# Performance work log

Hardware: AMD Instinct MI355X
Metric: run time of the kernel (lower is better)

Reference implementation:

```python
import jax, jax.numpy as jnp
import numpy as np

N = 3072
FEAT = 128
E = 24576


def setup_inputs() -> dict:
    key = jax.random.key(0)
    k1, k2, k3, k4 = jax.random.split(key, 4)
    x = jax.random.normal(k1, (N, FEAT), dtype=jnp.float32)
    edge_index = jax.random.randint(k2, (2, E), 0, N, dtype=jnp.int32)
    batch = jnp.zeros((N,), dtype=jnp.int32)
    # lin: Linear(2*FEAT, 1)
    w = jax.random.normal(k3, (2 * FEAT,), dtype=jnp.float32) / np.sqrt(2 * FEAT)
    b = jax.random.normal(k4, (), dtype=jnp.float32) * 0.01
    return {"x": x, "edge_index": edge_index, "batch": batch, "w": w, "b": b}


def _cc_labels(adj):
    """Connected-component labels via min-label propagation + pointer jumping.
    Labels equal the minimum node index of each component, so ranking them by
    value reproduces scipy's first-occurrence component ordering."""
    n = adj.shape[0]
    adj = jax.lax.stop_gradient(adj)

    def body(state):
        labels, _ = state
        neigh = jnp.where(adj > 0, labels[None, :], n).min(axis=1)  # [n]
        new = jnp.minimum(labels, neigh)
        new = jnp.minimum(new, new[new])  # pointer jumping
        return new, jnp.any(new != labels)

    labels, _ = jax.lax.while_loop(lambda s: s[1], body,
                                   (jnp.arange(n), jnp.array(True)))
    return labels


def reference(x, edge_index, batch, w, b):
    n, f = x.shape
    idx = jnp.arange(n)
    src, dst = edge_index[0], edge_index[1]
    # undirected: duplicate each edge in both directions (coalesce in the
    # original dedups; dense scatter-set below is equivalent since duplicate
    # (u,v) edges get identical scores)
    s2 = jnp.concatenate([src, dst])
    d2 = jnp.concatenate([dst, src])
    # per-edge raw score: lin(concat(x[u], x[v]))  ->  tanh
    e = jnp.tanh(x[s2] @ w[:f] + x[d2] @ w[f:] + b)  # [2E]

    zero = jnp.zeros((n, n), dtype=x.dtype)
    A = zero.at[s2, d2].set(1.0).at[idx, idx].set(0.0)   # self-loops removed
    S = zero.at[s2, d2].set(e).at[idx, idx].set(0.0)
    contract = (e > 0.0).astype(x.dtype)                 # tanh -> threshold 0
    A_c = zero.at[s2, d2].max(contract).at[idx, idx].set(0.0)

    labels = _cc_labels(A_c)                             # min-node-index labels
    roots = (labels == idx).astype(jnp.int32)
    cluster = (jnp.cumsum(roots) - 1)[labels]            # consecutive 0..K-1
    C = jax.nn.one_hot(cluster, n, dtype=x.dtype)        # [n, n] (padded to n)

    single = (A_c.sum(axis=1) + A_c.sum(axis=0)) == 0    # isolated under contraction
    S = S.at[idx, idx].set(single.astype(x.dtype))

    X_new = (S @ C).T @ x                                # [n(padK), f]
    A_new = (C.T @ A @ C).at[idx, idx].set(0.0)          # dense coarsened adjacency
    new_batch = jnp.zeros((n,), dtype=batch.dtype).at[cluster].max(batch)
    return X_new, A_new, new_batch, cluster
```

## Files before the change

kernel.cpp:

```cpp
#include <hip/hip_runtime.h>
#include <math.h>

#define N 3072
#define FEAT 128
#define NE 24576
#define PSTRIDE 64
#define EPT 24
#define NBLK 256
#define DOTB 768
#define OUTZ4 2459136
#define OUTZB 2402
#define WSZ4 1540
#define WSZB 2

__device__ __forceinline__ void wave_agg_add(bool valid, int key, float val,
                                             float* base, int stride, int off) {
    int lane = threadIdx.x & 63;
    unsigned long long active = __ballot(valid ? 1 : 0);
    while (active) {
        int leader = __ffsll(active) - 1;
        int lkey = __shfl(key, leader);
        bool mine = valid && (key == lkey);
        unsigned long long grp = __ballot(mine ? 1 : 0);
        float v = mine ? val : 0.0f;
        #pragma unroll
        for (int o = 32; o; o >>= 1) v += __shfl_xor(v, o);
        if (lane == leader)
            atomicAdd(&base[(size_t)lkey * stride + off], v);
        active &= ~grp;
    }
}

__device__ __forceinline__ void gsync(int* bar, int* lgen) {
    __syncthreads();
    if (threadIdx.x == 0) {
        __threadfence();
        int g = ++(*lgen);
        if (atomicAdd(&bar[0], 1) == (int)gridDim.x - 1) {
            __hip_atomic_store(&bar[0], 0, __ATOMIC_RELAXED, __HIP_MEMORY_SCOPE_AGENT);
            __threadfence();
            atomicAdd(&bar[1], 1);
        } else {
            while (__hip_atomic_load(&bar[1], __ATOMIC_RELAXED,
                                     __HIP_MEMORY_SCOPE_AGENT) < g)
                __builtin_amdgcn_s_sleep(8);
        }
        __threadfence();
    } else {
        ++(*lgen);
    }
    __syncthreads();
}

__global__ void k_init(const float* __restrict__ x, const float* __restrict__ w,
                       float* __restrict__ a, float* __restrict__ c,
                       float4* __restrict__ zout, float4* __restrict__ zws) {
    int b = blockIdx.x, t = threadIdx.x;
    if (b < DOTB) {
        int node = b * 4 + (t >> 6);
        int lane = t & 63;
        const float* xi = x + node * FEAT;
        float pa = xi[lane] * w[lane] + xi[lane + 64] * w[lane + 64];
        float pc = xi[lane] * w[FEAT + lane] + xi[lane + 64] * w[FEAT + lane + 64];
        for (int off = 32; off; off >>= 1) {
            pa += __shfl_down(pa, off);
            pc += __shfl_down(pc, off);
        }
        if (lane == 0) { a[node] = pa; c[node] = pc; }
    } else if (b < DOTB + OUTZB) {
        float4 z = {0.f, 0.f, 0.f, 0.f};
        int base = (b - DOTB) * 1024;
        #pragma unroll
        for (int k = 0; k < 4; ++k) {
            int idx = base + k * 256 + t;
            if (idx < OUTZ4) zout[idx] = z;
        }
    } else {
        float4 z = {0.f, 0.f, 0.f, 0.f};
        int base = (b - DOTB - OUTZB) * 1024;
        #pragma unroll
        for (int k = 0; k < 4; ++k) {
            int idx = base + k * 256 + t;
            if (idx < WSZ4) zws[idx] = z;
        }
    }
}

__global__ void __launch_bounds__(1024, 4)
k_mega(const int* __restrict__ ei, const float* __restrict__ x,
       const float* __restrict__ a, const float* __restrict__ c,
       const float* __restrict__ bb, int* __restrict__ bar,
       int* __restrict__ pcnt, int* __restrict__ notsingle,
       unsigned* __restrict__ ep, unsigned long long* __restrict__ qmask,
       float* __restrict__ y, unsigned long long* __restrict__ ptab,
       int* __restrict__ cluster, float* __restrict__ Xnew,
       float* __restrict__ Anew, float* __restrict__ out_cluster) {
    __shared__ int lab[N];
    __shared__ int ssum[1024];
    __shared__ unsigned short rk[N];
    __shared__ int sh_p[16 * 64];
    __shared__ int flag;
    int t = threadIdx.x, blk = blockIdx.x;
    int wv = t >> 6, lane = t & 63;
    int lgen = 0;

    if (t < 96) {
        int s = blk * 96 + t;
        int u = ei[s], v = ei[NE + s];
        unsigned wpk = (unsigned)u | ((unsigned)v << 12);
        if (u != v) {
            float b = bb[0];
            float su = a[u] + c[v] + b;
            float sv = a[v] + c[u] + b;
            unsigned fu = (su > 0.f) ? 1u : 0u;
            unsigned fv = (sv > 0.f) ? 1u : 0u;
            wpk |= (fu << 24) | (fv << 25);
            if (fu | fv) { notsingle[u] = 1; notsingle[v] = 1; }
            float eu = tanhf(su);
            int sl = atomicAdd(&pcnt[v], 1);
            if (sl < PSTRIDE)
                ptab[(size_t)v * PSTRIDE + sl] =
                    ((unsigned long long)__float_as_uint(eu) << 32) | (unsigned)u;
            float ev2 = tanhf(sv);
            sl = atomicAdd(&pcnt[u], 1);
            if (sl < PSTRIDE)
                ptab[(size_t)u * PSTRIDE + sl] =
                    ((unsigned long long)__float_as_uint(ev2) << 32) | (unsigned)v;
        }
        ep[s] = wpk;
    }
    gsync(bar, &lgen);

    if (blk == 0) {
        unsigned er[EPT];
        #pragma unroll
        for (int j = 0; j < EPT; ++j) er[j] = ep[t + j * 1024];
        for (int i = t; i < N; i += 1024) lab[i] = i;
        for (;;) {
            __syncthreads();
            if (t == 0) flag = 0;
            __syncthreads();
            #pragma unroll
            for (int j = 0; j < EPT; ++j) {
                unsigned wpk = er[j];
                int u = wpk & 0xFFF, v = (wpk >> 12) & 0xFFF;
                if (wpk & (1u << 24)) {
                    int lv = lab[v];
                    if (lv < lab[u]) { atomicMin(&lab[u], lv); flag = 1; }
                }
                if (wpk & (1u << 25)) {
                    int lu = lab[u];
                    if (lu < lab[v]) { atomicMin(&lab[v], lu); flag = 1; }
                }
            }
            for (int i = t; i < N; i += 1024) {
                int m = lab[i];
                int mm = lab[m];
                while (mm < m) { m = mm; mm = lab[m]; }
                if (m < lab[i]) { atomicMin(&lab[i], m); flag = 1; }
            }
            __syncthreads();
            if (!flag) break;
        }
        int i0 = 3 * t;
        int r0 = (lab[i0] == i0);
        int r1 = (lab[i0 + 1] == i0 + 1);
        int r2 = (lab[i0 + 2] == i0 + 2);
        int s = r0 + r1 + r2;
        ssum[t] = s;
        __syncthreads();
        for (int off = 1; off < 1024; off <<= 1) {
            int val = (t >= off) ? ssum[t - off] : 0;
            __syncthreads();
            ssum[t] += val;
            __syncthreads();
        }
        int run = ssum[t] - s;
        run += r0; rk[i0]     = (unsigned short)(run - 1);
        run += r1; rk[i0 + 1] = (unsigned short)(run - 1);
        run += r2; rk[i0 + 2] = (unsigned short)(run - 1);
        __syncthreads();
        for (int j = t; j < N; j += 1024) {
            int cl = rk[lab[j]];
            cluster[j] = cl;
            out_cluster[j] = (float)cl;
        }
    } else {
        int q = (blk - 1) * 16 + wv;
        if (q < N) {
            int cnt = pcnt[q]; if (cnt > PSTRIDE) cnt = PSTRIDE;
            const unsigned long long* row = ptab + (size_t)q * PSTRIDE;
            int myp = -1 - lane;
            float mye = 0.f;
            if (lane < cnt) {
                unsigned long long s = row[lane];
                myp = (int)(s & 0xFFFFFFFFu);
                mye = __uint_as_float((unsigned)(s >> 32));
            }
            sh_p[wv * 64 + lane] = myp;
            bool dup = false;
            for (int j = 0; j < lane && !dup; ++j)
                dup = (sh_p[wv * 64 + j] == myp);
            bool valid = (lane < cnt) && !dup;
            unsigned long long m = __ballot(valid ? 1 : 0);
            if (lane == 0) qmask[q] = m;
            float acc0 = 0.f, acc1 = 0.f;
            for (int j = 0; j < cnt; ++j) {
                if (!((m >> j) & 1ull)) continue;
                int p = __shfl(myp, j);
                float e = __shfl(mye, j);
                const float* xp = x + p * FEAT;
                acc0 += e * xp[lane];
                acc1 += e * xp[lane + 64];
            }
            if (!notsingle[q]) {
                const float* xq = x + q * FEAT;
                acc0 += xq[lane];
                acc1 += xq[lane + 64];
            }
            float* yq = y + q * FEAT;
            yq[lane] = acc0;
            yq[lane + 64] = acc1;
        }
    }
    gsync(bar, &lgen);

    for (int gw = blk * 16 + wv; gw < 9216; gw += NBLK * 16) {
        if (gw < 6144) {
            int f = gw & (FEAT - 1);
            int chunk = gw >> 7;
            int q = chunk * 64 + lane;
            wave_agg_add(true, cluster[q], y[q * FEAT + f], Xnew, FEAT, f);
        } else {
            int q = gw - 6144;
            int cnt = pcnt[q]; if (cnt > PSTRIDE) cnt = PSTRIDE;
            unsigned long long m = qmask[q];
            bool valid = (lane < cnt) && ((m >> lane) & 1ull);
            int p = 0;
            if (valid) p = (int)(ptab[(size_t)q * PSTRIDE + lane] & 0xFFFFFFFFu);
            int cq = cluster[q];
            int cp = valid ? cluster[p] : 0;
            valid = valid && (cp != cq);
            wave_agg_add(valid, cp * N + cq, 1.0f, Anew, 1, 0);
        }
    }
}

extern "C" void kernel_launch(void* const* d_in, const int* in_sizes, int n_in,
                              void* d_out, int out_size, void* d_ws, size_t ws_size,
                              hipStream_t stream) {
    const float* x  = (const float*)d_in[0];
    const int*   ei = (const int*)d_in[1];
    const float* w  = (const float*)d_in[3];
    const float* bb = (const float*)d_in[4];

    char* ws = (char*)d_ws;
    size_t off = 0;
    int* bar      = (int*)(ws + off);      off += 64;
    int* pcnt     = (int*)(ws + off);      off += (size_t)N * 4;
    int* notsing  = (int*)(ws + off);      off += (size_t)N * 4;
    float* a      = (float*)(ws + off);    off += (size_t)N * 4;
    float* c      = (float*)(ws + off);    off += (size_t)N * 4;
    int* cluster  = (int*)(ws + off);      off += (size_t)N * 4;
    unsigned* ep  = (unsigned*)(ws + off); off += (size_t)NE * 4;
    unsigned long long* qmask = (unsigned long long*)(ws + off); off += (size_t)N * 8;
    float* y      = (float*)(ws + off);    off += (size_t)N * FEAT * 4;
    unsigned long long* ptab = (unsigned long long*)(ws + off); off += (size_t)N * PSTRIDE * 8;

    float* Xnew        = (float*)d_out;
    float* Anew        = Xnew + (size_t)N * FEAT;
    float* out_cluster = Anew + (size_t)N * N + N;

    k_init<<<DOTB + OUTZB + WSZB, 256, 0, stream>>>(x, w, a, c,
                                                    (float4*)d_out, (float4*)ws);
    k_mega<<<NBLK, 1024, 0, stream>>>(ei, x, a, c, bb, bar, pcnt, notsing,
                                      ep, qmask, y, ptab, cluster,
                                      Xnew, Anew, out_cluster);
}
```

Before: 161.5 us.

## Split persistent megakernel into separate launches and overlap output zeroing with propagation

Removes the software grid barriers by splitting the persistent kernel into separate kernels for edge scoring, label propagation plus neighbor gather, and Xnew/Anew reduction. Output zeroing moves out of the init kernel into extra blocks of the propagation kernel, so it runs while the single-block label propagation is busy. The propagation loop now only visits contraction-active edges via a bitmask, and it drops edges and nodes once their labels reach zero. The cost is extra kernel launches and a more conservative register budget from the relaxed launch bounds.

```diff
diff --git a/kernel.cpp b/kernel.cpp
--- a/kernel.cpp
+++ b/kernel.cpp
@@ -6,12 +6,10 @@
 #define NE 24576
 #define PSTRIDE 64
 #define EPT 24
-#define NBLK 256
 #define DOTB 768
-#define OUTZ4 2459136
-#define OUTZB 2402
-#define WSZ4 1540
-#define WSZB 2
+#define OUTZ4 2458368
+#define ZB3 608
+#define GATB 192
 
 __device__ __forceinline__ void wave_agg_add(bool valid, int key, float val,
                                              float* base, int stride, int off) {
@@ -31,30 +29,9 @@
     }
 }
 
-__device__ __forceinline__ void gsync(int* bar, int* lgen) {
-    __syncthreads();
-    if (threadIdx.x == 0) {
-        __threadfence();
-        int g = ++(*lgen);
-        if (atomicAdd(&bar[0], 1) == (int)gridDim.x - 1) {
-            __hip_atomic_store(&bar[0], 0, __ATOMIC_RELAXED, __HIP_MEMORY_SCOPE_AGENT);
-            __threadfence();
-            atomicAdd(&bar[1], 1);
-        } else {
-            while (__hip_atomic_load(&bar[1], __ATOMIC_RELAXED,
-                                     __HIP_MEMORY_SCOPE_AGENT) < g)
-                __builtin_amdgcn_s_sleep(8);
-        }
-        __threadfence();
-    } else {
-        ++(*lgen);
-    }
-    __syncthreads();
-}
-
 __global__ void k_init(const float* __restrict__ x, const float* __restrict__ w,
                        float* __restrict__ a, float* __restrict__ c,
-                       float4* __restrict__ zout, float4* __restrict__ zws) {
+                       float4* __restrict__ zws) {
     int b = blockIdx.x, t = threadIdx.x;
     if (b < DOTB) {
         int node = b * 4 + (t >> 6);
@@ -67,34 +44,49 @@
             pc += __shfl_down(pc, off);
         }
         if (lane == 0) { a[node] = pa; c[node] = pc; }
-    } else if (b < DOTB + OUTZB) {
-        float4 z = {0.f, 0.f, 0.f, 0.f};
-        int base = (b - DOTB) * 1024;
-        #pragma unroll
-        for (int k = 0; k < 4; ++k) {
-            int idx = base + k * 256 + t;
-            if (idx < OUTZ4) zout[idx] = z;
-        }
     } else {
         float4 z = {0.f, 0.f, 0.f, 0.f};
-        int base = (b - DOTB - OUTZB) * 1024;
-        #pragma unroll
-        for (int k = 0; k < 4; ++k) {
-            int idx = base + k * 256 + t;
-            if (idx < WSZ4) zws[idx] = z;
-        }
-    }
-}
-
-__global__ void __launch_bounds__(1024, 4)
-k_mega(const int* __restrict__ ei, const float* __restrict__ x,
-       const float* __restrict__ a, const float* __restrict__ c,
-       const float* __restrict__ bb, int* __restrict__ bar,
-       int* __restrict__ pcnt, int* __restrict__ notsingle,
-       unsigned* __restrict__ ep, unsigned long long* __restrict__ qmask,
-       float* __restrict__ y, unsigned long long* __restrict__ ptab,
-       int* __restrict__ cluster, float* __restrict__ Xnew,
-       float* __restrict__ Anew, float* __restrict__ out_cluster) {
+        #pragma unroll
+        for (int k = 0; k < 6; ++k) zws[k * 256 + t] = z;
+    }
+}
+
+__global__ void k_edge_pairs(const int* __restrict__ ei, const float* __restrict__ a,
+                             const float* __restrict__ c, const float* __restrict__ bb,
+                             unsigned* __restrict__ ep, int* __restrict__ notsingle,
+                             int* __restrict__ pcnt, unsigned long long* __restrict__ ptab) {
+    int t = blockIdx.x * blockDim.x + threadIdx.x;
+    if (t >= NE) return;
+    int u = ei[t], v = ei[NE + t];
+    unsigned wpk = (unsigned)u | ((unsigned)v << 12);
+    if (u != v) {
+        float b = bb[0];
+        float su = a[u] + c[v] + b;
+        float sv = a[v] + c[u] + b;
+        unsigned fu = (su > 0.f) ? 1u : 0u;
+        unsigned fv = (sv > 0.f) ? 1u : 0u;
+        wpk |= (fu << 24) | (fv << 25);
+        if (fu | fv) { notsingle[u] = 1; notsingle[v] = 1; }
+        float eu = tanhf(su);
+        int sl = atomicAdd(&pcnt[v], 1);
+        if (sl < PSTRIDE)
+            ptab[(size_t)v * PSTRIDE + sl] =
+                ((unsigned long long)__float_as_uint(eu) << 32) | (unsigned)u;
+        float ev2 = tanhf(sv);
+        sl = atomicAdd(&pcnt[u], 1);
+        if (sl < PSTRIDE)
+            ptab[(size_t)u * PSTRIDE + sl] =
+                ((unsigned long long)__float_as_uint(ev2) << 32) | (unsigned)v;
+    }
+    ep[t] = wpk;
+}
+
+__global__ void __launch_bounds__(1024)
+k_prop_gather(const unsigned* __restrict__ ep, const float* __restrict__ x,
+              const int* __restrict__ pcnt, const unsigned long long* __restrict__ ptab,
+              const int* __restrict__ notsingle, float* __restrict__ y,
+              unsigned long long* __restrict__ qmask, int* __restrict__ cluster,
+              float* __restrict__ out_cluster, float4* __restrict__ zout) {
     __shared__ int lab[N];
     __shared__ int ssum[1024];
     __shared__ unsigned short rk[N];
@@ -102,59 +94,33 @@
     __shared__ int flag;
     int t = threadIdx.x, blk = blockIdx.x;
     int wv = t >> 6, lane = t & 63;
-    int lgen = 0;
-
-    if (t < 96) {
-        int s = blk * 96 + t;
-        int u = ei[s], v = ei[NE + s];
-        unsigned wpk = (unsigned)u | ((unsigned)v << 12);
-        if (u != v) {
-            float b = bb[0];
-            float su = a[u] + c[v] + b;
-            float sv = a[v] + c[u] + b;
-            unsigned fu = (su > 0.f) ? 1u : 0u;
-            unsigned fv = (sv > 0.f) ? 1u : 0u;
-            wpk |= (fu << 24) | (fv << 25);
-            if (fu | fv) { notsingle[u] = 1; notsingle[v] = 1; }
-            float eu = tanhf(su);
-            int sl = atomicAdd(&pcnt[v], 1);
-            if (sl < PSTRIDE)
-                ptab[(size_t)v * PSTRIDE + sl] =
-                    ((unsigned long long)__float_as_uint(eu) << 32) | (unsigned)u;
-            float ev2 = tanhf(sv);
-            sl = atomicAdd(&pcnt[u], 1);
-            if (sl < PSTRIDE)
-                ptab[(size_t)u * PSTRIDE + sl] =
-                    ((unsigned long long)__float_as_uint(ev2) << 32) | (unsigned)v;
-        }
-        ep[s] = wpk;
-    }
-    gsync(bar, &lgen);
-
     if (blk == 0) {
         unsigned er[EPT];
-        #pragma unroll
-        for (int j = 0; j < EPT; ++j) er[j] = ep[t + j * 1024];
+        unsigned act = 0;
+        #pragma unroll
+        for (int j = 0; j < EPT; ++j) {
+            er[j] = ep[t + j * 1024];
+            if (er[j] & 0x3000000u) act |= (1u << j);
+        }
         for (int i = t; i < N; i += 1024) lab[i] = i;
         for (;;) {
             __syncthreads();
             if (t == 0) flag = 0;
             __syncthreads();
-            #pragma unroll
-            for (int j = 0; j < EPT; ++j) {
+            unsigned rem = act;
+            while (rem) {
+                int j = __ffs(rem) - 1;
+                rem &= rem - 1;
                 unsigned wpk = er[j];
                 int u = wpk & 0xFFF, v = (wpk >> 12) & 0xFFF;
-                if (wpk & (1u << 24)) {
-                    int lv = lab[v];
-                    if (lv < lab[u]) { atomicMin(&lab[u], lv); flag = 1; }
-                }
-                if (wpk & (1u << 25)) {
-                    int lu = lab[u];
-                    if (lu < lab[v]) { atomicMin(&lab[v], lu); flag = 1; }
-                }
+                int lu = lab[u], lv = lab[v];
+                if ((lu | lv) == 0) { act &= ~(1u << j); continue; }
+                if ((wpk & (1u << 24)) && lv < lu) { atomicMin(&lab[u], lv); flag = 1; }
+                if ((wpk & (1u << 25)) && lu < lv) { atomicMin(&lab[v], lu); flag = 1; }
             }
             for (int i = t; i < N; i += 1024) {
                 int m = lab[i];
+                if (m == 0) continue;
                 int mm = lab[m];
                 while (mm < m) { m = mm; mm = lab[m]; }
                 if (m < lab[i]) { atomicMin(&lab[i], m); flag = 1; }
@@ -185,64 +151,75 @@
             cluster[j] = cl;
             out_cluster[j] = (float)cl;
         }
+    } else if (blk <= GATB) {
+        int q = (blk - 1) * 16 + wv;
+        int cnt = pcnt[q]; if (cnt > PSTRIDE) cnt = PSTRIDE;
+        const unsigned long long* row = ptab + (size_t)q * PSTRIDE;
+        int myp = -1 - lane;
+        float mye = 0.f;
+        if (lane < cnt) {
+            unsigned long long s = row[lane];
+            myp = (int)(s & 0xFFFFFFFFu);
+            mye = __uint_as_float((unsigned)(s >> 32));
+        }
+        sh_p[wv * 64 + lane] = myp;
+        bool dup = false;
+        for (int j = 0; j < lane && !dup; ++j)
+            dup = (sh_p[wv * 64 + j] == myp);
+        bool valid = (lane < cnt) && !dup;
+        unsigned long long m = __ballot(valid ? 1 : 0);
+        if (lane == 0) qmask[q] = m;
+        float acc0 = 0.f, acc1 = 0.f;
+        for (int j = 0; j < cnt; ++j) {
+            if (!((m >> j) & 1ull)) continue;
+            int p = __shfl(myp, j);
+            float e = __shfl(mye, j);
+            const float* xp = x + p * FEAT;
+            acc0 += e * xp[lane];
+            acc1 += e * xp[lane + 64];
+        }
+        if (!notsingle[q]) {
+            const float* xq = x + q * FEAT;
+            acc0 += xq[lane];
+            acc1 += xq[lane + 64];
+        }
+        float* yq = y + q * FEAT;
+        yq[lane] = acc0;
+        yq[lane + 64] = acc1;
     } else {
-        int q = (blk - 1) * 16 + wv;
-        if (q < N) {
-            int cnt = pcnt[q]; if (cnt > PSTRIDE) cnt = PSTRIDE;
-            const unsigned long long* row = ptab + (size_t)q * PSTRIDE;
-            int myp = -1 - lane;
-            float mye = 0.f;
-            if (lane < cnt) {
-                unsigned long long s = row[lane];
-                myp = (int)(s & 0xFFFFFFFFu);
-                mye = __uint_as_float((unsigned)(s >> 32));
-            }
-            sh_p[wv * 64 + lane] = myp;
-            bool dup = false;
-            for (int j = 0; j < lane && !dup; ++j)
-                dup = (sh_p[wv * 64 + j] == myp);
-            bool valid = (lane < cnt) && !dup;
-            unsigned long long m = __ballot(valid ? 1 : 0);
-            if (lane == 0) qmask[q] = m;
-            float acc0 = 0.f, acc1 = 0.f;
-            for (int j = 0; j < cnt; ++j) {
-                if (!((m >> j) & 1ull)) continue;
-                int p = __shfl(myp, j);
-                float e = __shfl(mye, j);
-                const float* xp = x + p * FEAT;
-                acc0 += e * xp[lane];
-                acc1 += e * xp[lane + 64];
-            }
-            if (!notsingle[q]) {
-                const float* xq = x + q * FEAT;
-                acc0 += xq[lane];
-                acc1 += xq[lane + 64];
-            }
-            float* yq = y + q * FEAT;
-            yq[lane] = acc0;
-            yq[lane + 64] = acc1;
-        }
-    }
-    gsync(bar, &lgen);
-
-    for (int gw = blk * 16 + wv; gw < 9216; gw += NBLK * 16) {
-        if (gw < 6144) {
-            int f = gw & (FEAT - 1);
-            int chunk = gw >> 7;
-            int q = chunk * 64 + lane;
-            wave_agg_add(true, cluster[q], y[q * FEAT + f], Xnew, FEAT, f);
-        } else {
-            int q = gw - 6144;
-            int cnt = pcnt[q]; if (cnt > PSTRIDE) cnt = PSTRIDE;
-            unsigned long long m = qmask[q];
-            bool valid = (lane < cnt) && ((m >> lane) & 1ull);
-            int p = 0;
-            if (valid) p = (int)(ptab[(size_t)q * PSTRIDE + lane] & 0xFFFFFFFFu);
-            int cq = cluster[q];
-            int cp = valid ? cluster[p] : 0;
-            valid = valid && (cp != cq);
-            wave_agg_add(valid, cp * N + cq, 1.0f, Anew, 1, 0);
-        }
+        float4 z = {0.f, 0.f, 0.f, 0.f};
+        int base = (blk - GATB - 1) * 4096;
+        #pragma unroll
+        for (int k = 0; k < 4; ++k) {
+            int idx = base + k * 1024 + t;
+            if (idx < OUTZ4) zout[idx] = z;
+        }
+    }
+}
+
+__global__ void k_reduce_anew(const float* __restrict__ y, const int* __restrict__ cluster,
+                              const int* __restrict__ pcnt,
+                              const unsigned long long* __restrict__ ptab,
+                              const unsigned long long* __restrict__ qmask,
+                              float* __restrict__ Xnew, float* __restrict__ Anew) {
+    int gid = blockIdx.x * blockDim.x + threadIdx.x;
+    int wid = gid >> 6, lane = gid & 63;
+    if (wid < 6144) {
+        int f = wid & (FEAT - 1);
+        int chunk = wid >> 7;
+        int q = chunk * 64 + lane;
+        wave_agg_add(true, cluster[q], y[q * FEAT + f], Xnew, FEAT, f);
+    } else {
+        int q = wid - 6144;
+        int cnt = pcnt[q]; if (cnt > PSTRIDE) cnt = PSTRIDE;
+        unsigned long long m = qmask[q];
+        bool valid = (lane < cnt) && ((m >> lane) & 1ull);
+        int p = 0;
+        if (valid) p = (int)(ptab[(size_t)q * PSTRIDE + lane] & 0xFFFFFFFFu);
+        int cq = cluster[q];
+        int cp = valid ? cluster[p] : 0;
+        valid = valid && (cp != cq);
+        wave_agg_add(valid, cp * N + cq, 1.0f, Anew, 1, 0);
     }
 }
 
@@ -256,7 +233,6 @@
 
     char* ws = (char*)d_ws;
     size_t off = 0;
-    int* bar      = (int*)(ws + off);      off += 64;
     int* pcnt     = (int*)(ws + off);      off += (size_t)N * 4;
     int* notsing  = (int*)(ws + off);      off += (size_t)N * 4;
     float* a      = (float*)(ws + off);    off += (size_t)N * 4;
@@ -271,9 +247,11 @@
     float* Anew        = Xnew + (size_t)N * FEAT;
     float* out_cluster = Anew + (size_t)N * N + N;
 
-    k_init<<<DOTB + OUTZB + WSZB, 256, 0, stream>>>(x, w, a, c,
-                                                    (float4*)d_out, (float4*)ws);
-    k_mega<<<NBLK, 1024, 0, stream>>>(ei, x, a, c, bb, bar, pcnt, notsing,
-                                      ep, qmask, y, ptab, cluster,
-                                      Xnew, Anew, out_cluster);
-}
+    k_init<<<DOTB + 1, 256, 0, stream>>>(x, w, a, c, (float4*)ws);
+    k_edge_pairs<<<NE / 256, 256, 0, stream>>>(ei, a, c, bb, ep, notsing, pcnt, ptab);
+    k_prop_gather<<<1 + GATB + ZB3, 1024, 0, stream>>>(ep, x, pcnt, ptab, notsing, y,
+                                                       qmask, cluster, out_cluster,
+                                                       (float4*)d_out);
+    k_reduce_anew<<<(9216 * 64) / 1024, 1024, 0, stream>>>(y, cluster, pcnt, ptab,
+                                                           qmask, Xnew, Anew);
+}
```

Measured after the change: 146.2 us. 1.1x faster.
